# Kernel tuning notes

Hardware: AMD Instinct MI355X
Metric: run time of the kernel (lower is better)

The kernel has to match this reference:

```python
import jax, jax.numpy as jnp
import numpy as np

SUBSTEPS = 2  # fixed RK4 substeps per save interval (replaces adaptive diffrax solver)


def setup_inputs() -> dict:
    key = jax.random.key(0)
    k = jax.random.split(key, 6)
    dim, hidden, neighbors, T = 512, 2048, 512, 9
    ts = jnp.linspace(0.0, 1.0, T, dtype=jnp.float32)
    y0 = jax.random.normal(k[0], (dim,), dtype=jnp.float32)
    Dy0 = jax.random.normal(k[1], (neighbors, dim), dtype=jnp.float32) * 0.01
    W1 = jax.random.normal(k[2], (dim, hidden), dtype=jnp.float32) / np.sqrt(dim).astype(np.float32)
    b1 = jax.random.normal(k[3], (hidden,), dtype=jnp.float32) * 0.01
    W2 = jax.random.normal(k[4], (hidden, dim), dtype=jnp.float32) / np.sqrt(hidden).astype(np.float32)
    b2 = jax.random.normal(k[5], (dim,), dtype=jnp.float32) * 0.01
    return {"ts": ts, "y0": y0, "Dy0": Dy0, "W1": W1, "b1": b1, "W2": W2, "b2": b2}


def reference(ts, y0, Dy0, W1, b1, W2, b2):
    tmap = jax.tree_util.tree_map

    def f(y):  # autonomous NeuralODE vector field: 2-layer tanh MLP
        return jnp.tanh(y @ W1 + b1) @ W2 + b2

    def rhs(u):
        y, Dy = u                      # y: [dim], Dy: [neighbors, dim]
        z = y + Dy                     # [neighbors, dim]

        def second_order(z_):          # per-neighbor, z_: [dim]
            def first_order(y_):
                return jax.jvp(f, (y_,), (z_ - y_,))
            (dy, dDy1), (_, dDy2) = jax.jvp(first_order, (y,), (z_ - y,))
            return dy, 1.5 * dDy1 + 0.5 * dDy2

        dy, dDy = jax.vmap(second_order, out_axes=(None, 0))(z)
        return (dy, dDy)

    def axpy(u, k, c):
        return tmap(lambda a, b: a + c * b, u, k)

    def rk4(u, dt):
        k1 = rhs(u)
        k2 = rhs(axpy(u, k1, dt * 0.5))
        k3 = rhs(axpy(u, k2, dt * 0.5))
        k4 = rhs(axpy(u, k3, dt))
        return tmap(lambda a, a1, a2, a3, a4: a + (dt / 6.0) * (a1 + 2.0 * a2 + 2.0 * a3 + a4),
                    u, k1, k2, k3, k4)

    def interval(u, tpair):
        t0, t1 = tpair
        dt = (t1 - t0) / SUBSTEPS
        def body(u_, _):
            return rk4(u_, dt), None
        u_new, _ = jax.lax.scan(body, u, None, length=SUBSTEPS)
        return u_new, u_new

    u0 = (y0, Dy0)
    _, (ys, Dys) = jax.lax.scan(interval, u0, (ts[:-1], ts[1:]))
    ys = jnp.concatenate([y0[None], ys], axis=0)        # [T, dim]
    Dys = jnp.concatenate([Dy0[None], Dys], axis=0)     # [T, neighbors, dim]
    # pack (y, Dy) trajectories into one array: [T, 1+neighbors, dim]
    return jnp.concatenate([ys[:, None, :], Dys], axis=1)
```

## Files before the change

### kernel.cpp

```cpp
#include <hip/hip_runtime.h>
#include <hip/hip_bf16.h>

typedef __attribute__((ext_vector_type(8))) short short8;
typedef float f32x4 __attribute__((ext_vector_type(4)));

#define DIM 512
#define HID 2048
#define ROWSZ (513*512)
#define DT 0.0625f

#define WAITV(n) asm volatile("s_waitcnt vmcnt(" #n ")" ::: "memory")
#define WAITL()  asm volatile("s_waitcnt lgkmcnt(0)" ::: "memory")
#define SBAR()   asm volatile("s_barrier" ::: "memory")
typedef const __attribute__((address_space(1))) void* gas1;
typedef __attribute__((address_space(3))) void* las3;
#define GLL16(g,l,aux) __builtin_amdgcn_global_load_lds((gas1)(g),(las3)(l),16,0,aux)
#define GLL4(g,l,aux)  __builtin_amdgcn_global_load_lds((gas1)(g),(las3)(l),4,0,aux)

__device__ __forceinline__ unsigned short f2bfu(float f){ __hip_bfloat16 h=__float2bfloat16(f); return *(unsigned short*)&h; }

__device__ __forceinline__ void xbar(int* arr, int* gen, int target, bool lead){
  asm volatile("s_waitcnt vmcnt(0) lgkmcnt(0)" ::: "memory");
  __syncthreads();
  if (threadIdx.x == 0){
    __hip_atomic_fetch_add(arr, 1, __ATOMIC_RELAXED, __HIP_MEMORY_SCOPE_AGENT);
    if (lead){
      while (__hip_atomic_load(arr, __ATOMIC_RELAXED, __HIP_MEMORY_SCOPE_AGENT) < 32*target)
        __builtin_amdgcn_s_sleep(2);
      __hip_atomic_store(gen, target, __ATOMIC_RELAXED, __HIP_MEMORY_SCOPE_AGENT);
    } else {
      while (__hip_atomic_load(gen, __ATOMIC_RELAXED, __HIP_MEMORY_SCOPE_AGENT) < target)
        __builtin_amdgcn_s_sleep(4);
    }
  }
  __syncthreads();
}

__device__ __forceinline__ void post_flag(int* f, int seq){
  asm volatile("s_waitcnt vmcnt(0) lgkmcnt(0)" ::: "memory");
  __syncthreads();
  if (threadIdx.x == 0)
    __hip_atomic_store(f, seq, __ATOMIC_RELAXED, __HIP_MEMORY_SCOPE_AGENT);
}
__device__ __forceinline__ void wait_flags32(int* base, int seq){
  if (threadIdx.x < 32){
    while (__hip_atomic_load(&base[threadIdx.x], __ATOMIC_RELAXED, __HIP_MEMORY_SCOPE_AGENT) < seq)
      __builtin_amdgcn_s_sleep(2);
  }
  __syncthreads();
}

__global__ void k_transpose_bf16(const float* __restrict__ src,
                                 __hip_bfloat16* __restrict__ dst, int R, int C) {
  __shared__ float tile[32][33];
  int c0 = blockIdx.x * 32, r0 = blockIdx.y * 32;
  int tx = threadIdx.x & 31, ty = threadIdx.x >> 5;
  for (int i = 0; i < 32; i += 8)
    tile[ty + i][tx] = src[(size_t)(r0 + ty + i) * C + c0 + tx];
  __syncthreads();
  for (int i = 0; i < 32; i += 8)
    dst[(size_t)(c0 + ty + i) * R + r0 + tx] = __float2bfloat16(tile[tx][ty + i]);
}

__global__ __launch_bounds__(512, 1) void k_persist(
    const float* __restrict__ y0, const float* __restrict__ Dy0,
    const unsigned short* __restrict__ W1t, const unsigned short* __restrict__ W2t,
    const float* __restrict__ b1, const float* __restrict__ b2,
    unsigned short* __restrict__ Vbuf, unsigned short* __restrict__ tbuf,
    float* __restrict__ yts, unsigned short* __restrict__ a_ss, float* __restrict__ pbuf,
    int* __restrict__ ctrl, float* __restrict__ out) {
  __shared__ __align__(16) short W1L[64 * 512];
  __shared__ __align__(16) short W2L[16 * 2048];
  __shared__ __align__(16) short ring[3][4096];
  __shared__ float ytL[DIM];
  __shared__ __align__(16) unsigned short ytB[DIM];
  __shared__ __align__(16) unsigned short asL[2048];
  __shared__ float pacc[64];
  __shared__ float c1L[64], c2L[64];
  __shared__ int bcast[2];

  const int t = threadIdx.x;
  if (t == 0) {
    int x;
    asm volatile("s_getreg_b32 %0, hwreg(HW_REG_XCC_ID)" : "=s"(x));
    x &= 7;
    bcast[0] = x;
    bcast[1] = atomicAdd(&ctrl[x], 1);
  }
  __syncthreads();
  const int xcd = bcast[0];
  const int sl  = bcast[1] & 31;
  const bool lead = (sl == 0);
  int* arr = ctrl + 64 + xcd * 64;
  int* gen = arr + 32;
  int* flgAb = ctrl + 704 + xcd * 32;
  int* flgBb = ctrl + 960 + xcd * 32;

  const int w = t >> 6, lane = t & 63, quad = lane >> 4, l16 = lane & 15;
  const int r8 = lane >> 3;
  const int mX = xcd * 64;
  const int nA = sl * 64;
  const int nB2 = sl * 16;
  float* ytx = yts + xcd * DIM;
  unsigned short* asx = a_ss + xcd * HID;

  const int awm = (w & 1) * 32, awn = (w >> 1) * 16;
  const int pj = w >> 1, ph = w & 1;

  const short8 z8 = {0,0,0,0,0,0,0,0};

  f32x4 DyR = {0.f,0.f,0.f,0.f}, K1 = DyR, K2 = DyR, K3 = DyR;
  float yR = 0.f, kd1 = 0.f, kd2 = 0.f, kd3 = 0.f;
  const int erow0 = mX + pj * 16 + quad * 4;
  const int ecol  = nB2 + l16;

  auto issueA = [&](int buf, int c) {
    int k0 = c * 64;
    GLL16(Vbuf + (size_t)(mX + w * 8 + r8) * DIM + k0 + (((lane & 7) ^ r8) << 3),
          &ring[buf][(w * 8) * 64], 1);
  };
  auto issueB = [&](int buf, int c) {
    int k0 = c * 64;
    GLL16(tbuf + (size_t)(mX + w * 8 + r8) * HID + k0 + (((lane & 7) ^ r8) << 3),
          &ring[buf][(w * 8) * 64], 1);
  };

#pragma unroll
  for (int i = 0; i < 8; ++i) {
    int r = w * 8 + i;
    int src = ((lane & ~7) | ((lane & 7) ^ (r & 7))) << 3;
    GLL16(W1t + (size_t)(nA + r) * DIM + src, &W1L[r * 512], 0);
  }
#pragma unroll
  for (int i = 0; i < 2; ++i) {
    int r = w * 2 + i;
#pragma unroll
    for (int j = 0; j < 4; ++j) {
      int g0 = j * 64 + lane;
      int src = ((g0 & ~7) | ((g0 & 7) ^ (r & 7))) << 3;
      GLL16(W2t + (size_t)(nB2 + r) * HID + src, &W2L[r * 2048 + j * 512], 0);
    }
  }
  if (!ph) {
#pragma unroll
    for (int r = 0; r < 4; ++r) {
      float v = Dy0[(size_t)(erow0 + r) * DIM + ecol];
      DyR[r] = v;
      Vbuf[(size_t)(erow0 + r) * DIM + ecol] = f2bfu(v);
      out[DIM + (size_t)(erow0 + r) * DIM + ecol] = v;
    }
  }
  if (t < 16) {
    float v = y0[nB2 + t];
    yR = v;
    ytx[nB2 + t] = v;
    if (xcd == 0) out[nB2 + t] = v;
  }
  WAITV(0);
  __syncthreads();
  xbar(arr, gen, 1, lead);

  for (int ss = 0; ss < 16; ++ss) {
    for (int st = 0; st < 4; ++st) {
      const float cn = (st == 2) ? DT : 0.5f * DT;
      const int seq = ss * 4 + st + 1;
      {
        wait_flags32(flgBb, seq - 1);
        GLL4(ytx + w * 64 + lane, &ytL[w * 64], 1);
        issueA(0, 0); issueA(1, 1);
        WAITV(2); SBAR();
        ytB[t] = f2bfu(ytL[t]);
        f32x4 acc0 = {0.f,0.f,0.f,0.f}, acc1 = acc0, acc2 = acc0;
        short8 ra0[2][2], ra1[2][2], rb[2][2], ya[2][2];
        const int pa0 = awm + l16, pa1 = awm + 16 + l16, pbW = awn + l16;
        WAITV(1); WAITL(); SBAR();
        {
          const short* tA = ring[0];
#pragma unroll
          for (int k2 = 0; k2 < 2; ++k2) {
            int lg = k2 * 4 + quad;
            ra0[0][k2] = *(const short8*)&tA[pa0 * 64 + ((lg ^ (pa0 & 7)) << 3)];
            ra1[0][k2] = *(const short8*)&tA[pa1 * 64 + ((lg ^ (pa1 & 7)) << 3)];
            int gb = lg;
            rb[0][k2] = *(const short8*)&W1L[pbW * 512 + (((gb & ~7) | ((gb & 7) ^ (pbW & 7))) << 3)];
            short8 yv = *(const short8*)&ytB[gb * 8];
            if (l16 != 0) yv = z8;
            ya[0][k2] = yv;
          }
        }
        WAITL();
#pragma unroll
        for (int c = 0; c < 8; ++c) {
          const int pr = c & 1, nx = pr ^ 1;
          if (c < 6)       { issueA((c + 2) % 3, c + 2); WAITV(1); }
          else if (c == 6) { WAITV(0); }
          if (c < 7) {
            SBAR();
            const short* tA = ring[(c + 1) % 3];
#pragma unroll
            for (int k2 = 0; k2 < 2; ++k2) {
              int lg = k2 * 4 + quad;
              ra0[nx][k2] = *(const short8*)&tA[pa0 * 64 + ((lg ^ (pa0 & 7)) << 3)];
              ra1[nx][k2] = *(const short8*)&tA[pa1 * 64 + ((lg ^ (pa1 & 7)) << 3)];
              int gb = (c + 1) * 8 + lg;
              rb[nx][k2] = *(const short8*)&W1L[pbW * 512 + (((gb & ~7) | ((gb & 7) ^ (pbW & 7))) << 3)];
              short8 yv = *(const short8*)&ytB[gb * 8];
              if (l16 != 0) yv = z8;
              ya[nx][k2] = yv;
            }
          }
#pragma unroll
          for (int k2 = 0; k2 < 2; ++k2) {
            acc0 = __builtin_amdgcn_mfma_f32_16x16x32_bf16(ra0[pr][k2], rb[pr][k2], acc0, 0, 0, 0);
            acc1 = __builtin_amdgcn_mfma_f32_16x16x32_bf16(ra1[pr][k2], rb[pr][k2], acc1, 0, 0, 0);
            acc2 = __builtin_amdgcn_mfma_f32_16x16x32_bf16(ya[pr][k2],  rb[pr][k2], acc2, 0, 0, 0);
          }
          if (c < 7) WAITL();
        }
        if ((w & 1) == 0 && quad == 0) pacc[awn + l16] = acc2[0];
        WAITL(); SBAR();
        if (t < 64) {
          float hsum = b1[nA + t] + pacc[t];
          float a = tanhf(hsum);
          float ap = 1.f - a * a;
          c1L[t] = ap; c2L[t] = -a * ap;
          asx[nA + t] = f2bfu(a);
        }
        WAITL(); SBAR();
        int row0 = mX + awm + quad * 4;
        int coln = nA + awn + l16;
        float C1 = c1L[awn + l16], C2 = c2L[awn + l16];
#pragma unroll
        for (int r = 0; r < 4; ++r) {
          float g0 = acc0[r], g1 = acc1[r];
          tbuf[(size_t)(row0 + r) * HID + coln]      = f2bfu(g0 * (C1 + C2 * g0));
          tbuf[(size_t)(row0 + 16 + r) * HID + coln] = f2bfu(g1 * (C1 + C2 * g1));
        }
        post_flag(&flgAb[sl], seq);
      }
      {
        wait_flags32(flgAb, seq);
        GLL4((const unsigned short*)asx + w * 128 + lane * 2, &asL[w * 128], 1);
        GLL4((const unsigned short*)asx + 1024 + w * 128 + lane * 2, &asL[1024 + w * 128], 1);
        issueB(0, 0); issueB(1, 1);
        WAITV(2); SBAR();
        f32x4 acc = {0.f,0.f,0.f,0.f}, acc2 = acc;
        const int paB = pj * 16 + l16;
        const int lgW = ph * 4 + quad;
#pragma unroll
        for (int c = 0; c < 32; ++c) {
          if (c < 31) { WAITV(1); } else { WAITV(0); }
          SBAR();
          if (c < 30) issueB((c + 2) % 3, c + 2);
          const short* tA = ring[c % 3];
          short8 a = *(const short8*)&tA[paB * 64 + ((lgW ^ (paB & 7)) << 3)];
          int gb = c * 8 + lgW;
          short8 b = *(const short8*)&W2L[l16 * 2048 + (((gb & ~7) | ((gb & 7) ^ (l16 & 7))) << 3)];
          short8 av = *(const short8*)&asL[gb * 8];
          if (l16 != 0) av = z8;
          acc  = __builtin_amdgcn_mfma_f32_16x16x32_bf16(a,  b, acc,  0, 0, 0);
          acc2 = __builtin_amdgcn_mfma_f32_16x16x32_bf16(av, b, acc2, 0, 0, 0);
        }
        float* red = (float*)&ring[0][0];
        if (ph) {
#pragma unroll
          for (int r = 0; r < 4; ++r) red[pj * 256 + (quad * 4 + r) * 16 + l16] = acc[r];
          if (w == 1 && quad == 0) red[1024 + l16] = acc2[0];
        }
        WAITL(); SBAR();
        if (!ph) {
          f32x4 o;
#pragma unroll
          for (int r = 0; r < 4; ++r) o[r] = acc[r] + red[pj * 256 + (quad * 4 + r) * 16 + l16];
          if (st == 0) K1 = o; else if (st == 1) K2 = o; else if (st == 2) K3 = o;
          if (st < 3) {
#pragma unroll
            for (int r = 0; r < 4; ++r) {
              float v = DyR[r] + cn * o[r];
              Vbuf[(size_t)(erow0 + r) * DIM + ecol] = f2bfu(v);
            }
          } else {
            const float dt6 = DT / 6.f;
#pragma unroll
            for (int r = 0; r < 4; ++r) {
              float v = DyR[r] + dt6 * (K1[r] + 2.f * K2[r] + 2.f * K3[r] + o[r]);
              DyR[r] = v;
              Vbuf[(size_t)(erow0 + r) * DIM + ecol] = f2bfu(v);
              if (ss & 1) out[(size_t)(ss / 2 + 1) * ROWSZ + DIM + (size_t)(erow0 + r) * DIM + ecol] = v;
            }
          }
        }
        if (t < 16) {
          float k4 = acc2[0] + red[1024 + t] + b2[nB2 + t];
          if (st == 0) kd1 = k4; else if (st == 1) kd2 = k4; else if (st == 2) kd3 = k4;
          if (st < 3) {
            ytx[nB2 + t] = yR + cn * k4;
          } else {
            yR += (DT / 6.f) * (kd1 + 2.f * kd2 + 2.f * kd3 + k4);
            ytx[nB2 + t] = yR;
            if ((ss & 1) && xcd == 0) out[(size_t)(ss / 2 + 1) * ROWSZ + nB2 + t] = yR;
          }
        }
        post_flag(&flgBb[sl], seq);
      }
    }
  }
}

extern "C" void kernel_launch(void* const* d_in, const int* in_sizes, int n_in,
                              void* d_out, int out_size, void* d_ws, size_t ws_size,
                              hipStream_t stream) {
  const float* y0  = (const float*)d_in[1];
  const float* Dy0 = (const float*)d_in[2];
  const float* W1  = (const float*)d_in[3];
  const float* b1  = (const float*)d_in[4];
  const float* W2  = (const float*)d_in[5];
  const float* b2  = (const float*)d_in[6];
  float* out = (float*)d_out;

  char* p = (char*)d_ws;
  auto alloc = [&](size_t bytes) {
    char* r = p;
    p += (bytes + 255) & ~(size_t)255;
    return r;
  };
  unsigned short* W1t  = (unsigned short*)alloc((size_t)HID * DIM * 2);
  unsigned short* W2t  = (unsigned short*)alloc((size_t)DIM * HID * 2);
  unsigned short* Vbuf = (unsigned short*)alloc((size_t)DIM * DIM * 2);
  unsigned short* tbuf = (unsigned short*)alloc((size_t)DIM * HID * 2);
  float* yts  = (float*)alloc(8 * DIM * 4);
  unsigned short* a_ss = (unsigned short*)alloc(8 * HID * 2);
  float* pbuf = (float*)alloc((size_t)8 * 16 * 2112 * 4);
  int* ctrl   = (int*)alloc(8192);

  hipMemsetAsync(ctrl, 0, 8192, stream);
  k_transpose_bf16<<<dim3(HID / 32, DIM / 32), 256, 0, stream>>>(W1, (__hip_bfloat16*)W1t, DIM, HID);
  k_transpose_bf16<<<dim3(DIM / 32, HID / 32), 256, 0, stream>>>(W2, (__hip_bfloat16*)W2t, HID, DIM);
  k_persist<<<256, 512, 0, stream>>>(y0, Dy0, W1t, W2t, b1, b2,
                                     Vbuf, tbuf, yts, a_ss, pbuf, ctrl, out);
}
```

Before: 731.9 us.

## Replace full flag barrier with staged per-group polling in second GEMM

Instead of waiting for all 32 producer flags before the W2 GEMM phase, each wave polls only the 8 flags covering the next K-quarter and loads the matching slice of the activation vector just in time. The pipeline wait counts are adjusted at the poll points to account for the extra asL loads. This lets consumption of early tbuf chunks overlap with producers still finishing later chunks, at the cost of more polling and a trickier vmcnt accounting.

```diff
diff --git a/kernel.cpp b/kernel.cpp
--- a/kernel.cpp
+++ b/kernel.cpp
@@ -48,6 +48,14 @@
       __builtin_amdgcn_s_sleep(2);
   }
   __syncthreads();
+}
+__device__ __forceinline__ void group_poll8(int* base, int seq){
+  const int idx = threadIdx.x & 7;
+  while (true){
+    int v = __hip_atomic_load(&base[idx], __ATOMIC_RELAXED, __HIP_MEMORY_SCOPE_AGENT);
+    if (__all(v >= seq)) break;
+    __builtin_amdgcn_s_sleep(1);
+  }
 }
 
 __global__ void k_transpose_bf16(const float* __restrict__ src,
@@ -124,6 +132,12 @@
     GLL16(tbuf + (size_t)(mX + w * 8 + r8) * HID + k0 + (((lane & 7) ^ r8) << 3),
           &ring[buf][(w * 8) * 64], 1);
   };
+  auto issueAsl = [&](int q) {
+#pragma unroll
+    for (int j = 0; j < 4; ++j)
+      GLL4((const unsigned short*)asx + q * 512 + j * 128 + lane * 2,
+           &asL[q * 512 + j * 128], 1);
+  };
 
 #pragma unroll
   for (int i = 0; i < 8; ++i) {
@@ -239,19 +253,31 @@
         post_flag(&flgAb[sl], seq);
       }
       {
-        wait_flags32(flgAb, seq);
-        GLL4((const unsigned short*)asx + w * 128 + lane * 2, &asL[w * 128], 1);
-        GLL4((const unsigned short*)asx + 1024 + w * 128 + lane * 2, &asL[1024 + w * 128], 1);
+        group_poll8(flgAb, seq);
+        issueAsl(0);
         issueB(0, 0); issueB(1, 1);
-        WAITV(2); SBAR();
         f32x4 acc = {0.f,0.f,0.f,0.f}, acc2 = acc;
         const int paB = pj * 16 + l16;
         const int lgW = ph * 4 + quad;
 #pragma unroll
         for (int c = 0; c < 32; ++c) {
-          if (c < 31) { WAITV(1); } else { WAITV(0); }
+          if (c == 6 || c == 14 || c == 22) {
+            group_poll8(flgAb + (c + 2), seq);
+            WAITV(0);
+          } else if (c == 7 || c == 15 || c == 23) {
+            WAITV(6);
+          } else if (c == 31) {
+            WAITV(0);
+          } else {
+            WAITV(1);
+          }
           SBAR();
-          if (c < 30) issueB((c + 2) % 3, c + 2);
+          if (c == 6 || c == 14 || c == 22) {
+            issueAsl((c + 2) >> 3);
+            issueB((c + 2) % 3, c + 2);
+          } else if (c < 30) {
+            issueB((c + 2) % 3, c + 2);
+          }
           const short* tA = ring[c % 3];
           short8 a = *(const short8*)&tA[paB * 64 + ((lgW ^ (paB & 7)) << 3)];
           int gb = c * 8 + lgW;
```

After: 850.4 us. 1.16x slower.

## Re-partition phase-B GEMM warps into 32-row tiles with 4-way K split

Applied to the files above, without the earlier changes.

The second-layer GEMM stage changes its work split across the 8 warps. Each warp now computes two 16-row M tiles that share one B fragment, so each W2 load feeds two MFMAs. K is split four ways by chunk parity and half-chunk, and the partial sums are reduced through LDS by the lead warp of each M pair. This is meant to cut redundant W2 LDS reads, at the cost of a larger 4-way reduction, a wider accumulator register footprint, and warps that skip every other K chunk.

```diff
diff --git a/kernel.cpp b/kernel.cpp
--- a/kernel.cpp
+++ b/kernel.cpp
@@ -105,14 +105,19 @@
   unsigned short* asx = a_ss + xcd * HID;
 
   const int awm = (w & 1) * 32, awn = (w >> 1) * 16;
-  const int pj = w >> 1, ph = w & 1;
+  const int mpB  = w >> 2;
+  const int khB  = (w >> 1) & 1;
+  const int parB = w & 1;
+  const int kpB  = w & 3;
 
   const short8 z8 = {0,0,0,0,0,0,0,0};
 
-  f32x4 DyR = {0.f,0.f,0.f,0.f}, K1 = DyR, K2 = DyR, K3 = DyR;
+  f32x4 DyR0 = {0.f,0.f,0.f,0.f}, DyR1 = DyR0;
+  f32x4 K1a = DyR0, K1b = DyR0, K2a = DyR0, K2b = DyR0, K3a = DyR0, K3b = DyR0;
   float yR = 0.f, kd1 = 0.f, kd2 = 0.f, kd3 = 0.f;
-  const int erow0 = mX + pj * 16 + quad * 4;
-  const int ecol  = nB2 + l16;
+  const int erowB0 = mX + mpB * 32 + quad * 4;
+  const int erowB1 = mX + mpB * 32 + 16 + quad * 4;
+  const int ecolB  = nB2 + l16;
 
   auto issueA = [&](int buf, int c) {
     int k0 = c * 64;
@@ -141,13 +146,17 @@
       GLL16(W2t + (size_t)(nB2 + r) * HID + src, &W2L[r * 2048 + j * 512], 0);
     }
   }
-  if (!ph) {
+  if (kpB == 0) {
 #pragma unroll
     for (int r = 0; r < 4; ++r) {
-      float v = Dy0[(size_t)(erow0 + r) * DIM + ecol];
-      DyR[r] = v;
-      Vbuf[(size_t)(erow0 + r) * DIM + ecol] = f2bfu(v);
-      out[DIM + (size_t)(erow0 + r) * DIM + ecol] = v;
+      float v0 = Dy0[(size_t)(erowB0 + r) * DIM + ecolB];
+      DyR0[r] = v0;
+      Vbuf[(size_t)(erowB0 + r) * DIM + ecolB] = f2bfu(v0);
+      out[DIM + (size_t)(erowB0 + r) * DIM + ecolB] = v0;
+      float v1 = Dy0[(size_t)(erowB1 + r) * DIM + ecolB];
+      DyR1[r] = v1;
+      Vbuf[(size_t)(erowB1 + r) * DIM + ecolB] = f2bfu(v1);
+      out[DIM + (size_t)(erowB1 + r) * DIM + ecolB] = v1;
     }
   }
   if (t < 16) {
@@ -244,54 +253,71 @@
         GLL4((const unsigned short*)asx + 1024 + w * 128 + lane * 2, &asL[1024 + w * 128], 1);
         issueB(0, 0); issueB(1, 1);
         WAITV(2); SBAR();
-        f32x4 acc = {0.f,0.f,0.f,0.f}, acc2 = acc;
-        const int paB = pj * 16 + l16;
-        const int lgW = ph * 4 + quad;
+        f32x4 acc0 = {0.f,0.f,0.f,0.f}, acc1 = acc0, acc2 = acc0;
+        const int ra0 = mpB * 32 + l16, ra1 = mpB * 32 + 16 + l16;
+        const int lg = khB * 4 + quad;
 #pragma unroll
         for (int c = 0; c < 32; ++c) {
           if (c < 31) { WAITV(1); } else { WAITV(0); }
           SBAR();
           if (c < 30) issueB((c + 2) % 3, c + 2);
-          const short* tA = ring[c % 3];
-          short8 a = *(const short8*)&tA[paB * 64 + ((lgW ^ (paB & 7)) << 3)];
-          int gb = c * 8 + lgW;
-          short8 b = *(const short8*)&W2L[l16 * 2048 + (((gb & ~7) | ((gb & 7) ^ (l16 & 7))) << 3)];
-          short8 av = *(const short8*)&asL[gb * 8];
-          if (l16 != 0) av = z8;
-          acc  = __builtin_amdgcn_mfma_f32_16x16x32_bf16(a,  b, acc,  0, 0, 0);
-          acc2 = __builtin_amdgcn_mfma_f32_16x16x32_bf16(av, b, acc2, 0, 0, 0);
-        }
-        float* red = (float*)&ring[0][0];
-        if (ph) {
-#pragma unroll
-          for (int r = 0; r < 4; ++r) red[pj * 256 + (quad * 4 + r) * 16 + l16] = acc[r];
-          if (w == 1 && quad == 0) red[1024 + l16] = acc2[0];
+          if ((c & 1) == parB) {
+            const short* tA = ring[c % 3];
+            short8 a0 = *(const short8*)&tA[ra0 * 64 + ((lg ^ (ra0 & 7)) << 3)];
+            short8 a1 = *(const short8*)&tA[ra1 * 64 + ((lg ^ (ra1 & 7)) << 3)];
+            int gb = c * 8 + lg;
+            short8 b = *(const short8*)&W2L[l16 * 2048 + (((gb & ~7) | ((gb & 7) ^ (l16 & 7))) << 3)];
+            acc0 = __builtin_amdgcn_mfma_f32_16x16x32_bf16(a0, b, acc0, 0, 0, 0);
+            acc1 = __builtin_amdgcn_mfma_f32_16x16x32_bf16(a1, b, acc1, 0, 0, 0);
+            if (mpB == 0) {
+              short8 av = *(const short8*)&asL[gb * 8];
+              if (l16 != 0) av = z8;
+              acc2 = __builtin_amdgcn_mfma_f32_16x16x32_bf16(av, b, acc2, 0, 0, 0);
+            }
+          }
+        }
+        float* redM = (float*)&ring[(mpB == 0) ? 0 : 2][0];
+        if (kpB) {
+          *(f32x4*)&redM[(0 * 3 + (kpB - 1)) * 256 + l16 * 16 + quad * 4] = acc0;
+          *(f32x4*)&redM[(1 * 3 + (kpB - 1)) * 256 + l16 * 16 + quad * 4] = acc1;
+          if (mpB == 0 && quad == 0) redM[1536 + (kpB - 1) * 16 + l16] = acc2[0];
         }
         WAITL(); SBAR();
-        if (!ph) {
-          f32x4 o;
-#pragma unroll
-          for (int r = 0; r < 4; ++r) o[r] = acc[r] + red[pj * 256 + (quad * 4 + r) * 16 + l16];
-          if (st == 0) K1 = o; else if (st == 1) K2 = o; else if (st == 2) K3 = o;
+        if (!kpB) {
+          f32x4 o0 = acc0, o1 = acc1;
+#pragma unroll
+          for (int p = 0; p < 3; ++p) {
+            o0 += *(const f32x4*)&redM[(0 * 3 + p) * 256 + l16 * 16 + quad * 4];
+            o1 += *(const f32x4*)&redM[(1 * 3 + p) * 256 + l16 * 16 + quad * 4];
+          }
+          if (st == 0)      { K1a = o0; K1b = o1; }
+          else if (st == 1) { K2a = o0; K2b = o1; }
+          else if (st == 2) { K3a = o0; K3b = o1; }
           if (st < 3) {
 #pragma unroll
             for (int r = 0; r < 4; ++r) {
-              float v = DyR[r] + cn * o[r];
-              Vbuf[(size_t)(erow0 + r) * DIM + ecol] = f2bfu(v);
+              Vbuf[(size_t)(erowB0 + r) * DIM + ecolB] = f2bfu(DyR0[r] + cn * o0[r]);
+              Vbuf[(size_t)(erowB1 + r) * DIM + ecolB] = f2bfu(DyR1[r] + cn * o1[r]);
             }
           } else {
             const float dt6 = DT / 6.f;
 #pragma unroll
             for (int r = 0; r < 4; ++r) {
-              float v = DyR[r] + dt6 * (K1[r] + 2.f * K2[r] + 2.f * K3[r] + o[r]);
-              DyR[r] = v;
-              Vbuf[(size_t)(erow0 + r) * DIM + ecol] = f2bfu(v);
-              if (ss & 1) out[(size_t)(ss / 2 + 1) * ROWSZ + DIM + (size_t)(erow0 + r) * DIM + ecol] = v;
+              float v0 = DyR0[r] + dt6 * (K1a[r] + 2.f * K2a[r] + 2.f * K3a[r] + o0[r]);
+              DyR0[r] = v0;
+              Vbuf[(size_t)(erowB0 + r) * DIM + ecolB] = f2bfu(v0);
+              float v1 = DyR1[r] + dt6 * (K1b[r] + 2.f * K2b[r] + 2.f * K3b[r] + o1[r]);
+              DyR1[r] = v1;
+              Vbuf[(size_t)(erowB1 + r) * DIM + ecolB] = f2bfu(v1);
+              if (ss & 1) {
+                out[(size_t)(ss / 2 + 1) * ROWSZ + DIM + (size_t)(erowB0 + r) * DIM + ecolB] = v0;
+                out[(size_t)(ss / 2 + 1) * ROWSZ + DIM + (size_t)(erowB1 + r) * DIM + ecolB] = v1;
+              }
             }
           }
         }
         if (t < 16) {
-          float k4 = acc2[0] + red[1024 + t] + b2[nB2 + t];
+          float k4 = acc2[0] + redM[1536 + t] + redM[1536 + 16 + t] + redM[1536 + 32 + t] + b2[nB2 + t];
           if (st == 0) kd1 = k4; else if (st == 1) kd2 = k4; else if (st == 2) kd3 = k4;
           if (st < 3) {
             ytx[nB2 + t] = yR + cn * k4;
```

Measured after the change: 884.9 us. 1.21x slower.

## Keep W1 B-fragments in registers and compute tanh coefficients per lane

Applied to the files above, without the earlier changes.

Each warp now loads its W1 column fragments once into registers (rbR[8][2]) and no longer stages W1 in shared memory or reads it per chunk. The hidden pre-activation is broadcast across lanes with a shuffle, so every lane computes tanh and its derivative coefficients itself. This removes the pacc/c1L/c2L shared arrays and two barriers per stage. It adds 64 VGPRs of persistent fragments, which raises register pressure and risks spills.

```diff
diff --git a/kernel.cpp b/kernel.cpp
--- a/kernel.cpp
+++ b/kernel.cpp
@@ -69,14 +69,11 @@
     unsigned short* __restrict__ Vbuf, unsigned short* __restrict__ tbuf,
     float* __restrict__ yts, unsigned short* __restrict__ a_ss, float* __restrict__ pbuf,
     int* __restrict__ ctrl, float* __restrict__ out) {
-  __shared__ __align__(16) short W1L[64 * 512];
   __shared__ __align__(16) short W2L[16 * 2048];
   __shared__ __align__(16) short ring[3][4096];
   __shared__ float ytL[DIM];
   __shared__ __align__(16) unsigned short ytB[DIM];
   __shared__ __align__(16) unsigned short asL[2048];
-  __shared__ float pacc[64];
-  __shared__ float c1L[64], c2L[64];
   __shared__ int bcast[2];
 
   const int t = threadIdx.x;
@@ -125,11 +122,15 @@
           &ring[buf][(w * 8) * 64], 1);
   };
 
-#pragma unroll
-  for (int i = 0; i < 8; ++i) {
-    int r = w * 8 + i;
-    int src = ((lane & ~7) | ((lane & 7) ^ (r & 7))) << 3;
-    GLL16(W1t + (size_t)(nA + r) * DIM + src, &W1L[r * 512], 0);
+  const float b1v = b1[nA + awn + l16];
+  short8 rbR[8][2];
+  {
+    const unsigned short* wrow = W1t + (size_t)(nA + awn + l16) * DIM;
+#pragma unroll
+    for (int c = 0; c < 8; ++c)
+#pragma unroll
+      for (int k2 = 0; k2 < 2; ++k2)
+        rbR[c][k2] = *(const short8*)&wrow[(c * 8 + k2 * 4 + quad) * 8];
   }
 #pragma unroll
   for (int i = 0; i < 2; ++i) {
@@ -171,8 +172,8 @@
         WAITV(2); SBAR();
         ytB[t] = f2bfu(ytL[t]);
         f32x4 acc0 = {0.f,0.f,0.f,0.f}, acc1 = acc0, acc2 = acc0;
-        short8 ra0[2][2], ra1[2][2], rb[2][2], ya[2][2];
-        const int pa0 = awm + l16, pa1 = awm + 16 + l16, pbW = awn + l16;
+        short8 ra0[2][2], ra1[2][2], ya[2][2];
+        const int pa0 = awm + l16, pa1 = awm + 16 + l16;
         WAITV(1); WAITL(); SBAR();
         {
           const short* tA = ring[0];
@@ -181,9 +182,7 @@
             int lg = k2 * 4 + quad;
             ra0[0][k2] = *(const short8*)&tA[pa0 * 64 + ((lg ^ (pa0 & 7)) << 3)];
             ra1[0][k2] = *(const short8*)&tA[pa1 * 64 + ((lg ^ (pa1 & 7)) << 3)];
-            int gb = lg;
-            rb[0][k2] = *(const short8*)&W1L[pbW * 512 + (((gb & ~7) | ((gb & 7) ^ (pbW & 7))) << 3)];
-            short8 yv = *(const short8*)&ytB[gb * 8];
+            short8 yv = *(const short8*)&ytB[lg * 8];
             if (l16 != 0) yv = z8;
             ya[0][k2] = yv;
           }
@@ -203,7 +202,6 @@
               ra0[nx][k2] = *(const short8*)&tA[pa0 * 64 + ((lg ^ (pa0 & 7)) << 3)];
               ra1[nx][k2] = *(const short8*)&tA[pa1 * 64 + ((lg ^ (pa1 & 7)) << 3)];
               int gb = (c + 1) * 8 + lg;
-              rb[nx][k2] = *(const short8*)&W1L[pbW * 512 + (((gb & ~7) | ((gb & 7) ^ (pbW & 7))) << 3)];
               short8 yv = *(const short8*)&ytB[gb * 8];
               if (l16 != 0) yv = z8;
               ya[nx][k2] = yv;
@@ -211,25 +209,19 @@
           }
 #pragma unroll
           for (int k2 = 0; k2 < 2; ++k2) {
-            acc0 = __builtin_amdgcn_mfma_f32_16x16x32_bf16(ra0[pr][k2], rb[pr][k2], acc0, 0, 0, 0);
-            acc1 = __builtin_amdgcn_mfma_f32_16x16x32_bf16(ra1[pr][k2], rb[pr][k2], acc1, 0, 0, 0);
-            acc2 = __builtin_amdgcn_mfma_f32_16x16x32_bf16(ya[pr][k2],  rb[pr][k2], acc2, 0, 0, 0);
+            acc0 = __builtin_amdgcn_mfma_f32_16x16x32_bf16(ra0[pr][k2], rbR[c][k2], acc0, 0, 0, 0);
+            acc1 = __builtin_amdgcn_mfma_f32_16x16x32_bf16(ra1[pr][k2], rbR[c][k2], acc1, 0, 0, 0);
+            acc2 = __builtin_amdgcn_mfma_f32_16x16x32_bf16(ya[pr][k2],  rbR[c][k2], acc2, 0, 0, 0);
           }
           if (c < 7) WAITL();
         }
-        if ((w & 1) == 0 && quad == 0) pacc[awn + l16] = acc2[0];
-        WAITL(); SBAR();
-        if (t < 64) {
-          float hsum = b1[nA + t] + pacc[t];
-          float a = tanhf(hsum);
-          float ap = 1.f - a * a;
-          c1L[t] = ap; c2L[t] = -a * ap;
-          asx[nA + t] = f2bfu(a);
-        }
-        WAITL(); SBAR();
+        float hval = __shfl(acc2[0], l16);
+        float av = tanhf(hval + b1v);
+        float ap = 1.f - av * av;
+        const float C1 = ap, C2 = -av * ap;
+        if ((w & 1) == 0 && quad == 0) asx[nA + awn + l16] = f2bfu(av);
         int row0 = mX + awm + quad * 4;
         int coln = nA + awn + l16;
-        float C1 = c1L[awn + l16], C2 = c2L[awn + l16];
 #pragma unroll
         for (int r = 0; r < 4; ++r) {
           float g0 = acc0[r], g1 = acc1[r];
```

Result: slower. 778.7 us (+6.4%).
